# Kernel tuning notes

Hardware: AMD Instinct MI355X
Metric: run time of the kernel (lower is better)

## Reference

```python
import jax, jax.numpy as jnp
import numpy as np

N = 100000            # number of nodes
E = 1600000           # number of edges (avg degree 16)
D = 32                # embedding dim
MASK_DEPTH = 3        # cfg.mask_depth
PATH_PROB = 0.5       # cfg.path_prob
NUM_MASK_CAND = 1024  # cfg.num_mask_cand
EPS_NORM = 1e-12      # F.normalize eps


def setup_inputs() -> dict:
    key = jax.random.key(0)
    k1, k2 = jax.random.split(key)
    edge_index = jax.random.randint(k1, (2, E), 0, N)  # [2, E] (row, col) COO indices
    adj_values = jnp.ones((E,), dtype=jnp.float32)     # sparse values (binary adjacency)
    embeds = jax.random.normal(k2, (N, D), dtype=jnp.float32)
    return {"edge_index": edge_index, "adj_values": adj_values, "embeds": embeds}


def _spmm(rows, cols, vals, x):
    # out[i] = sum_{e: rows[e]==i} vals[e] * x[cols[e]]  -- irregular gather + scatter-add
    return jax.ops.segment_sum(x[cols] * vals[:, None], rows, num_segments=N)


def _l2_normalize(x):
    n = jnp.sqrt(jnp.sum(x * x, axis=-1, keepdims=True))
    return x / jnp.maximum(n, EPS_NORM)


def reference(edge_index, adj_values, embeds):
    rows, cols = edge_index[0], edge_index[1]
    vals = adj_values

    # order = row-sums of sparse adj, shape [N, 1]
    order = jax.ops.segment_sum(vals, rows, num_segments=N)[:, None]

    fst_emb = _spmm(rows, cols, vals, embeds) - embeds
    fst_num = order
    emb = [fst_emb]
    num = [fst_num]

    drop_key = jax.random.key(42)
    for i in range(MASK_DEPTH):
        # sparse_dropout with keep prob path_prob**(i+1); zeroing values == dropping edges in spmm
        keep_prob = PATH_PROB ** (i + 1)
        u = jax.random.uniform(jax.random.fold_in(drop_key, i), (E,))
        keep = jnp.floor(u + keep_prob)  # 1.0 with prob keep_prob, else 0.0
        vals = vals * keep               # dropout compounds across iterations

        emb.append(_spmm(rows, cols, vals, emb[-1]) - emb[-1] - order * emb[-1])
        num.append(_spmm(rows, cols, vals, num[-1]) - num[-1] - order)
        order = jax.ops.segment_sum(vals, rows, num_segments=N)[:, None]

    subgraph_embeds = sum(emb) / (sum(num) + 1e-8)
    subgraph_embeds = _l2_normalize(subgraph_embeds)
    embeds_n = _l2_normalize(embeds)

    scores = jnp.sum(subgraph_embeds * embeds_n, axis=-1)  # [N]
    # Gumbel noise: -log(-log(U))
    u = jax.random.uniform(jax.random.key(7), (N,))
    scores = scores + (-jnp.log(-jnp.log(u)))

    _, candidates = jax.lax.top_k(scores, NUM_MASK_CAND)
    return scores, candidates
```

## Files before the change

### kernel.cpp

```cpp
#include <hip/hip_runtime.h>
#include <stdint.h>
#include <stddef.h>

#define NN 100000
#define NE 1600000
#define DD 32
#define NCAND 1024
#define HSIZE 65536
#define SORTN 4096
#define NBUK ((NN + 255) / 256)
#define EPB 4096
#define BCAP 5120
#define BCAPL 4608
#define CHK 5

#define CAP1 832000
#define CAP2 432000
#define CAP3 240000

__host__ __device__ inline void tf2x32(uint32_t k0, uint32_t k1, uint32_t x0, uint32_t x1,
                                       uint32_t& o0, uint32_t& o1) {
  uint32_t ks2 = k0 ^ k1 ^ 0x1BD11BDAu;
  uint32_t v0 = x0 + k0, v1 = x1 + k1;
#define TFR(r) { v0 += v1; v1 = (v1 << (r)) | (v1 >> (32 - (r))); v1 ^= v0; }
  TFR(13) TFR(15) TFR(26) TFR(6)   v0 += k1;  v1 += ks2 + 1u;
  TFR(17) TFR(29) TFR(16) TFR(24)  v0 += ks2; v1 += k0 + 2u;
  TFR(13) TFR(15) TFR(26) TFR(6)   v0 += k0;  v1 += k1 + 3u;
  TFR(17) TFR(29) TFR(16) TFR(24)  v0 += k1;  v1 += ks2 + 4u;
  TFR(13) TFR(15) TFR(26) TFR(6)   v0 += ks2; v1 += k0 + 5u;
#undef TFR
  o0 = v0; o1 = v1;
}

__device__ __forceinline__ uint32_t jax_bits32(uint32_t k0, uint32_t k1, uint32_t i) {
  uint32_t o0, o1;
  tf2x32(k0, k1, 0u, i, o0, o1);
  return o0 ^ o1;
}

__device__ __forceinline__ float bits_to_uniform(uint32_t b) {
  return __fsub_rn(__uint_as_float((b >> 9) | 0x3f800000u), 1.0f);
}

__device__ __forceinline__ float pw32c(float4 c0, float4 c1, float4 c2, float4 c3,
                                       float4 c4, float4 c5, float4 c6, float4 c7) {
  float r0 = __fadd_rn(__fadd_rn(__fadd_rn(c0.x, c2.x), c4.x), c6.x);
  float r1 = __fadd_rn(__fadd_rn(__fadd_rn(c0.y, c2.y), c4.y), c6.y);
  float r2 = __fadd_rn(__fadd_rn(__fadd_rn(c0.z, c2.z), c4.z), c6.z);
  float r3 = __fadd_rn(__fadd_rn(__fadd_rn(c0.w, c2.w), c4.w), c6.w);
  float r4 = __fadd_rn(__fadd_rn(__fadd_rn(c1.x, c3.x), c5.x), c7.x);
  float r5 = __fadd_rn(__fadd_rn(__fadd_rn(c1.y, c3.y), c5.y), c7.y);
  float r6 = __fadd_rn(__fadd_rn(__fadd_rn(c1.z, c3.z), c5.z), c7.z);
  float r7 = __fadd_rn(__fadd_rn(__fadd_rn(c1.w, c3.w), c5.w), c7.w);
  float a01 = __fadd_rn(r0, r1), a23 = __fadd_rn(r2, r3);
  float a45 = __fadd_rn(r4, r5), a67 = __fadd_rn(r6, r7);
  return __fadd_rn(__fadd_rn(a01, a23), __fadd_rn(a45, a67));
}

__device__ __forceinline__ float4 f4div1(float4 a, float d) {
  return make_float4(__fdiv_rn(a.x, d), __fdiv_rn(a.y, d),
                     __fdiv_rn(a.z, d), __fdiv_rn(a.w, d));
}
__device__ __forceinline__ float4 f4sq(float4 a) {
  return make_float4(__fmul_rn(a.x, a.x), __fmul_rn(a.y, a.y),
                     __fmul_rn(a.z, a.z), __fmul_rn(a.w, a.w));
}
__device__ __forceinline__ float4 f4dd(float4 s, float n1, float4 e, float n2) {
  return make_float4(__fmul_rn(__fdiv_rn(s.x, n1), __fdiv_rn(e.x, n2)),
                     __fmul_rn(__fdiv_rn(s.y, n1), __fdiv_rn(e.y, n2)),
                     __fmul_rn(__fdiv_rn(s.z, n1), __fdiv_rn(e.z, n2)),
                     __fmul_rn(__fdiv_rn(s.w, n1), __fdiv_rn(e.w, n2)));
}

__global__ __launch_bounds__(1024) void kA2_bin(
    const int* __restrict__ rows, const int* __restrict__ cols,
    const float* __restrict__ adj,
    uint32_t k00, uint32_t k01, uint32_t k10, uint32_t k11,
    uint32_t k20, uint32_t k21,
    int* __restrict__ bucketCursor, int4* __restrict__ pkBin,
    int* __restrict__ bucketCntS) {
  __shared__ int hist[NBUK];
  __shared__ int base[NBUK];
  __shared__ int h1[NBUK];
  __shared__ int h2[NBUK];
  __shared__ int h3[NBUK];
  __shared__ uint8_t lvs[EPB];
  __shared__ uint16_t rank16[EPB];
  int tid = threadIdx.x;
  for (int i = tid; i < NBUK; i += 1024) { hist[i] = 0; h1[i] = 0; h2[i] = 0; h3[i] = 0; }
  __syncthreads();
  int e0 = blockIdx.x * EPB;
#pragma unroll
  for (int k = 0; k < 4; ++k) {
    int e = e0 + k * 1024 + tid;
    int lv = 0;
    if (e < NE) {
      float u0 = bits_to_uniform(jax_bits32(k00, k01, (uint32_t)e));
      float u1 = bits_to_uniform(jax_bits32(k10, k11, (uint32_t)e));
      float u2 = bits_to_uniform(jax_bits32(k20, k21, (uint32_t)e));
      float kp0 = floorf(__fadd_rn(u0, 0.5f));
      float kp1 = floorf(__fadd_rn(u1, 0.25f));
      float kp2 = floorf(__fadd_rn(u2, 0.125f));
      if (kp0 != 0.0f) { lv = 1; if (kp1 != 0.0f) { lv = 2; if (kp2 != 0.0f) lv = 3; } }
      int b = rows[e] >> 8;
      rank16[k * 1024 + tid] = (uint16_t)atomicAdd(&hist[b], 1);
      if (lv >= 1) {
        atomicAdd(&h1[b], 1);
        if (lv >= 2) {
          atomicAdd(&h2[b], 1);
          if (lv >= 3) atomicAdd(&h3[b], 1);
        }
      }
    }
    lvs[k * 1024 + tid] = (uint8_t)lv;
  }
  __syncthreads();
  for (int i = tid; i < NBUK; i += 1024) {
    int h = hist[i];
    base[i] = (h > 0) ? atomicAdd(&bucketCursor[i], h) : 0;
    if (h1[i]) atomicAdd(&bucketCntS[i], h1[i]);
    if (h2[i]) atomicAdd(&bucketCntS[NBUK + i], h2[i]);
    if (h3[i]) atomicAdd(&bucketCntS[2 * NBUK + i], h3[i]);
  }
  __syncthreads();
#pragma unroll
  for (int k = 0; k < 4; ++k) {
    int e = e0 + k * 1024 + tid;
    if (e < NE) {
      int r = rows[e];
      int b = r >> 8;
      int lv = (int)lvs[k * 1024 + tid];
      int pos = base[b] + (int)rank16[k * 1024 + tid];
      if (pos < BCAP)
        pkBin[(size_t)b * BCAP + pos] =
            make_int4(cols[e], __float_as_int(adj[e]), (e << 2) | lv, r);
    }
  }
}

__global__ __launch_bounds__(512) void k_scanBS(const int* __restrict__ bucketCursor,
                                                const int* __restrict__ bucketCntS,
                                                int* __restrict__ bucketBaseS) {
  __shared__ int sb[512];
  int a = blockIdx.x;
  const int* c = (a == 0) ? bucketCursor : (bucketCntS + (size_t)(a - 1) * NBUK);
  int* o = bucketBaseS + (size_t)a * (NBUK + 1);
  int tid = threadIdx.x;
  int v = (tid < NBUK) ? c[tid] : 0;
  sb[tid] = v;
  __syncthreads();
  for (int off = 1; off < 512; off <<= 1) {
    int x = (tid >= off) ? sb[tid - off] : 0;
    __syncthreads();
    sb[tid] += x;
    __syncthreads();
  }
  if (tid < NBUK) o[tid] = sb[tid] - v;
  if (tid == NBUK - 1) o[NBUK] = sb[tid];
}

__global__ __launch_bounds__(1024) void kB_emit(
    const int* __restrict__ bucketBaseS, const int4* __restrict__ pkBin,
    int* __restrict__ rpAll,
    int2* __restrict__ pk0, int2* __restrict__ pk1,
    int2* __restrict__ pk2, int2* __restrict__ pk3,
    float* __restrict__ order0, float* __restrict__ order1, float* __restrict__ order2) {
  __shared__ unsigned long long cnt64[256];
  __shared__ unsigned long long scan64[1024];
  __shared__ int start0[256];
  __shared__ int cur[256];
  __shared__ uint32_t keyF[BCAPL];
  __shared__ uint32_t keyG[BCAPL];
  __shared__ uint16_t origG[BCAPL];
  int b = blockIdx.x, tid = threadIdx.x;
  int bB0 = bucketBaseS[b];
  int n = bucketBaseS[b + 1] - bB0;
  if (n > BCAPL) n = BCAPL;
  size_t sRead = (size_t)b * BCAP;
  const int* pkI = (const int*)pkBin;
  const int2* pkZW = (const int2*)pkBin;
  int r0 = b << 8;
  int nr = NN - r0; if (nr > 256) nr = 256;
  int bB1 = bucketBaseS[(NBUK + 1) + b];
  int bB2 = bucketBaseS[2 * (NBUK + 1) + b];
  int bB3 = bucketBaseS[3 * (NBUK + 1) + b];
  if (tid < 256) { cnt64[tid] = 0ull; cur[tid] = 0; }
  __syncthreads();
  for (int i = tid; i < n; i += 1024) {
    int2 zw = pkZW[2 * (sRead + (size_t)i) + 1];
    int lr = zw.y - r0;
    int lv = zw.x & 3;
    keyF[i] = ((uint32_t)lr << 23) | (uint32_t)zw.x;
    unsigned long long add = 1ull;
    if (lv >= 1) add |= 1ull << 16;
    if (lv >= 2) add |= 1ull << 32;
    if (lv >= 3) add |= 1ull << 48;
    atomicAdd(&cnt64[lr], add);
  }
  __syncthreads();
  unsigned long long own = (tid < 256) ? cnt64[tid] : 0ull;
  if (tid < 256) scan64[tid] = own;
  __syncthreads();
  for (int off = 1; off < 256; off <<= 1) {
    unsigned long long v = (tid < 256 && tid >= off) ? scan64[tid - off] : 0ull;
    __syncthreads();
    if (tid < 256) scan64[tid] += v;
    __syncthreads();
  }
  if (tid < 256) {
    unsigned long long ex = scan64[tid] - own;
    start0[tid] = (int)(ex & 0xFFFFull);
    if (tid < nr) {
      rpAll[r0 + tid] = bB0 + (int)(ex & 0xFFFFull);
      rpAll[(NN + 1) + r0 + tid] = bB1 + (int)((ex >> 16) & 0xFFFFull);
      rpAll[2 * (NN + 1) + r0 + tid] = bB2 + (int)((ex >> 32) & 0xFFFFull);
      rpAll[3 * (NN + 1) + r0 + tid] = bB3 + (int)((ex >> 48) & 0xFFFFull);
    }
  }
  if (b == NBUK - 1 && tid == 0) {
    rpAll[NN] = bucketBaseS[NBUK];
    rpAll[(NN + 1) + NN] = bucketBaseS[(NBUK + 1) + NBUK];
    rpAll[2 * (NN + 1) + NN] = bucketBaseS[2 * (NBUK + 1) + NBUK];
    rpAll[3 * (NN + 1) + NN] = bucketBaseS[3 * (NBUK + 1) + NBUK];
  }
  __syncthreads();
  for (int i = tid; i < n; i += 1024) {
    uint32_t k = keyF[i];
    int lr = (int)(k >> 23);
    int slot = start0[lr] + atomicAdd(&cur[lr], 1);
    origG[slot] = (uint16_t)i;
    keyG[slot] = k;
  }
  __syncthreads();
  int C2 = (n + 1023) >> 10;
  {
    int lo2 = tid * C2, hi2 = lo2 + C2;
    if (lo2 > n) lo2 = n;
    if (hi2 > n) hi2 = n;
    uint16_t vals[CHK];
    uint16_t pos[CHK];
    uint32_t keys[CHK];
#pragma unroll
    for (int q = 0; q < CHK; ++q) {
      int i = lo2 + q;
      if (i < hi2) {
        uint32_t ki = keyG[i];
        int lr = (int)(ki >> 23);
        int st = start0[lr];
        int d = (int)(cnt64[lr] & 0xFFFFull);
        int rank = 0;
        for (int j = 0; j < d; ++j) rank += (keyG[st + j] < ki) ? 1 : 0;
        vals[q] = origG[i];
        keys[q] = ki;
        pos[q] = (uint16_t)(st + rank);
      }
    }
    __syncthreads();
#pragma unroll
    for (int q = 0; q < CHK; ++q) {
      int i = lo2 + q;
      if (i < hi2) { origG[pos[q]] = vals[q]; keyG[pos[q]] = keys[q]; }
    }
  }
  __syncthreads();
  uint32_t* adjS = keyF;
  {
    uint32_t av[CHK];
#pragma unroll
    for (int q = 0; q < CHK; ++q) {
      int i = tid + q * 1024;
      if (i < n) av[q] = (uint32_t)pkI[4 * (sRead + (size_t)origG[i]) + 1];
    }
#pragma unroll
    for (int q = 0; q < CHK; ++q) {
      int i = tid + q * 1024;
      if (i < n) adjS[i] = av[q];
    }
  }
  __syncthreads();
  if (tid < nr) {
    int d = (int)(cnt64[tid] & 0xFFFFull);
    int st = start0[tid];
    float o0 = 0.0f, o1v = 0.0f, o2v = 0.0f;
    for (int i = 0; i < d; ++i) {
      int lv = (int)(keyG[st + i] & 3u);
      float a = __uint_as_float(adjS[st + i]);
      o0 = __fadd_rn(o0, a);
      if (lv >= 1) { o1v = __fadd_rn(o1v, a); if (lv >= 2) o2v = __fadd_rn(o2v, a); }
    }
    order0[r0 + tid] = o0; order1[r0 + tid] = o1v; order2[r0 + tid] = o2v;
  }
  int lo = tid * C2, hi = lo + C2;
  if (lo > n) lo = n;
  if (hi > n) hi = n;
  int c1 = 0, c2 = 0, c3 = 0;
  for (int i = lo; i < hi; ++i) {
    int lv = (int)(keyG[i] & 3u);
    c1 += (lv >= 1); c2 += (lv >= 2); c3 += (lv >= 3);
  }
  unsigned long long mine = (unsigned long long)c1 |
                            ((unsigned long long)c2 << 16) |
                            ((unsigned long long)c3 << 32);
  scan64[tid] = mine;
  __syncthreads();
  for (int off = 1; off < 1024; off <<= 1) {
    unsigned long long v = (tid >= off) ? scan64[tid - off] : 0ull;
    __syncthreads();
    scan64[tid] += v;
    __syncthreads();
  }
  unsigned long long ex = scan64[tid] - mine;
  int o1 = bB1 + (int)(ex & 0xFFFFull);
  int o2 = bB2 + (int)((ex >> 16) & 0xFFFFull);
  int o3 = bB3 + (int)((ex >> 32) & 0xFFFFull);
  {
    int colr[CHK];
#pragma unroll
    for (int q = 0; q < CHK; ++q) {
      int i = lo + q;
      if (i < hi) colr[q] = pkI[4 * (sRead + (size_t)origG[i])];
    }
#pragma unroll
    for (int q = 0; q < CHK; ++q) {
      int i = lo + q;
      if (i < hi) {
        int lv = (int)(keyG[i] & 3u);
        int2 pkv = make_int2(colr[q], (int)adjS[i]);
        pk0[bB0 + i] = pkv;
        if (lv >= 1) {
          pk1[o1++] = pkv;
          if (lv >= 2) {
            pk2[o2++] = pkv;
            if (lv >= 3) pk3[o3++] = pkv;
          }
        }
      }
    }
  }
}


__global__ void k_emb0(const int* __restrict__ rp, const int2* __restrict__ pk,
                       const float* __restrict__ embeds, float* __restrict__ e0) {
  int tid = blockIdx.x * blockDim.x + threadIdx.x;
  int r = tid >> 5, d = tid & 31;
  if (r >= NN) return;
  int s = rp[r], t = rp[r + 1];
  float acc = 0.0f;
  for (int base = s; base < t; base += 32) {
    int idx = base + d;
    int2 p = (idx < t) ? pk[idx] : make_int2(0, 0);
    int m = t - base; if (m > 32) m = 32;
    for (int j = 0; j < m; j += 8) {
      int cc[8], aa[8];
      float xx[8];
#pragma unroll
      for (int q = 0; q < 8; ++q) {
        cc[q] = __shfl(p.x, j + q, 32);
        aa[q] = __shfl(p.y, j + q, 32);
      }
#pragma unroll
      for (int q = 0; q < 8; ++q) xx[q] = embeds[(size_t)cc[q] * DD + d];
#pragma unroll
      for (int q = 0; q < 8; ++q)
        acc = __fadd_rn(acc, __fmul_rn(__int_as_float(aa[q]), xx[q]));
    }
  }
  e0[(size_t)r * DD + d] = __fsub_rn(acc, embeds[(size_t)r * DD + d]);
}

__global__ void k_emb_step(const int* __restrict__ rp, const int2* __restrict__ pk,
                           const float* __restrict__ ord, const float* __restrict__ ecur,
                           float* __restrict__ enext, float* __restrict__ esum,
                           const float* __restrict__ ncur, float* __restrict__ nnext,
                           float* __restrict__ nsum, int mode) {
  int tid = blockIdx.x * blockDim.x + threadIdx.x;
  int r = tid >> 5, d = tid & 31;
  if (r >= NN) return;
  int s = rp[r], t = rp[r + 1];
  float acc = 0.0f, accn = 0.0f;
  for (int base = s; base < t; base += 32) {
    int idx = base + d;
    int2 p = (idx < t) ? pk[idx] : make_int2(0, 0);
    int m = t - base; if (m > 32) m = 32;
    for (int j = 0; j < m; j += 8) {
      int cc[8], aa[8];
      float xx[8], nn[8];
#pragma unroll
      for (int q = 0; q < 8; ++q) {
        cc[q] = __shfl(p.x, j + q, 32);
        aa[q] = __shfl(p.y, j + q, 32);
      }
#pragma unroll
      for (int q = 0; q < 8; ++q) {
        xx[q] = ecur[(size_t)cc[q] * DD + d];
        nn[q] = ncur[cc[q]];
      }
#pragma unroll
      for (int q = 0; q < 8; ++q) {
        float av = __int_as_float(aa[q]);
        acc = __fadd_rn(acc, __fmul_rn(av, xx[q]));
        accn = __fadd_rn(accn, __fmul_rn(av, nn[q]));
      }
    }
  }
  float ordv = ord[r];
  size_t idx = (size_t)r * DD + d;
  float ec = ecur[idx];
  float o = __fsub_rn(__fsub_rn(acc, ec), __fmul_rn(ordv, ec));
  if (mode != 3) enext[idx] = o;
  if (mode == 1) esum[idx] = __fadd_rn(ec, o);
  else esum[idx] = __fadd_rn(esum[idx], o);
  if (d == 0) {
    float nc = ncur[r];
    float on = __fsub_rn(__fsub_rn(accn, nc), ordv);
    if (mode != 3) nnext[r] = on;
    if (mode == 1) nsum[r] = __fadd_rn(nc, on);
    else nsum[r] = __fadd_rn(nsum[r], on);
  }
}

__global__ __launch_bounds__(256) void k_final(
    const float* __restrict__ embeds, const float* __restrict__ emb_sum,
    const float* __restrict__ num_sum, uint32_t gk0, uint32_t gk1,
    float* __restrict__ out_scores, int* __restrict__ hist) {
  __shared__ uint32_t hb[512];
  __shared__ uint32_t hc[512];
  int r = blockIdx.x * blockDim.x + threadIdx.x;
  for (int i = threadIdx.x; i < 512; i += 256) { hb[i] = 0xFFFFFFFFu; hc[i] = 0u; }
  __syncthreads();
  if (r < NN) {
    float denom = __fadd_rn(num_sum[r], 1e-8f);
    const float4* ps = (const float4*)(emb_sum + (size_t)r * DD);
    const float4* pe = (const float4*)(embeds + (size_t)r * DD);
    float4 m0 = pe[0], m1 = pe[1], m2 = pe[2], m3 = pe[3],
           m4 = pe[4], m5 = pe[5], m6 = pe[6], m7 = pe[7];
    float4 s0 = f4div1(ps[0], denom), s1 = f4div1(ps[1], denom),
           s2 = f4div1(ps[2], denom), s3 = f4div1(ps[3], denom),
           s4 = f4div1(ps[4], denom), s5 = f4div1(ps[5], denom),
           s6 = f4div1(ps[6], denom), s7 = f4div1(ps[7], denom);
    float n1 = fmaxf(__fsqrt_rn(pw32c(f4sq(s0), f4sq(s1), f4sq(s2), f4sq(s3),
                                      f4sq(s4), f4sq(s5), f4sq(s6), f4sq(s7))), 1e-12f);
    float n2 = fmaxf(__fsqrt_rn(pw32c(f4sq(m0), f4sq(m1), f4sq(m2), f4sq(m3),
                                      f4sq(m4), f4sq(m5), f4sq(m6), f4sq(m7))), 1e-12f);
    float dot = pw32c(f4dd(s0, n1, m0, n2), f4dd(s1, n1, m1, n2),
                      f4dd(s2, n1, m2, n2), f4dd(s3, n1, m3, n2),
                      f4dd(s4, n1, m4, n2), f4dd(s5, n1, m5, n2),
                      f4dd(s6, n1, m6, n2), f4dd(s7, n1, m7, n2));
    float u = bits_to_uniform(jax_bits32(gk0, gk1, (uint32_t)r));
    float l1 = (float)log((double)u);
    float w = -l1;
    float l2 = (float)log((double)w);
    float g = -l2;
    float score = __fadd_rn(dot, g);
    out_scores[r] = score;
    uint32_t kb = __float_as_uint(score);
    kb = (kb & 0x80000000u) ? ~kb : (kb | 0x80000000u);
    uint32_t key = kb >> 16;
    uint32_t slot = (key * 2654435761u) >> 23;
    for (;;) {
      uint32_t prev = atomicCAS(&hb[slot], 0xFFFFFFFFu, key);
      if (prev == 0xFFFFFFFFu || prev == key) { atomicAdd(&hc[slot], 1u); break; }
      slot = (slot + 1) & 511u;
    }
  }
  __syncthreads();
  for (int i = threadIdx.x; i < 512; i += 256)
    if (hb[i] != 0xFFFFFFFFu) atomicAdd(&hist[hb[i]], (int)hc[i]);
}

__global__ void k_cutoff(const int* __restrict__ hist, int* __restrict__ cutoff) {
  __shared__ int psum[1024];
  int t = threadIdx.x;
  int base = HSIZE - (t + 1) * 64;
  int own = 0;
  for (int i = 0; i < 64; ++i) own += hist[base + i];
  psum[t] = own;
  __syncthreads();
  for (int off = 1; off < 1024; off <<= 1) {
    int v = (t >= off) ? psum[t - off] : 0;
    __syncthreads();
    psum[t] += v;
    __syncthreads();
  }
  int incl = psum[t];
  int prev = incl - own;
  if (incl >= NCAND && prev < NCAND) {
    int c = prev;
    int b = HSIZE - t * 64 - 1;
    while (b >= base) {
      c += hist[b];
      if (c >= NCAND) break;
      --b;
    }
    *cutoff = b;
  }
}

__global__ void k_collect(const float* __restrict__ scores, const int* __restrict__ cutoff,
                          unsigned long long* __restrict__ buf, int* __restrict__ cnt2) {
  int r = blockIdx.x * blockDim.x + threadIdx.x;
  if (r >= NN) return;
  uint32_t kb = __float_as_uint(scores[r]);
  kb = (kb & 0x80000000u) ? ~kb : (kb | 0x80000000u);
  if ((int)(kb >> 16) >= *cutoff) {
    int p = atomicAdd(cnt2, 1);
    if (p < SORTN)
      buf[p] = ((unsigned long long)kb << 32) | (uint32_t)(~(uint32_t)r);
  }
}

__global__ __launch_bounds__(256) void k_rank(const unsigned long long* __restrict__ buf,
                                              const int* __restrict__ cnt2,
                                              float* __restrict__ out_cand) {
  __shared__ unsigned long long s[SORTN];
  int m = *cnt2;
  if (m > SORTN) m = SORTN;
  if (blockIdx.x * 256 >= m) return;
  for (int i = threadIdx.x; i < m; i += 256) s[i] = buf[i];
  __syncthreads();
  int i = blockIdx.x * 256 + threadIdx.x;
  if (i >= m) return;
  unsigned long long mine = s[i];
  int rank = 0;
  int j = 0;
  for (; j + 8 <= m; j += 8) {
#pragma unroll
    for (int q = 0; q < 8; ++q) rank += (s[j + q] > mine) ? 1 : 0;
  }
  for (; j < m; ++j) rank += (s[j] > mine) ? 1 : 0;
  if (rank < NCAND) {
    uint32_t idx = ~((uint32_t)(mine & 0xffffffffull));
    out_cand[rank] = (float)idx;
  }
}

extern "C" void kernel_launch(void* const* d_in, const int* in_sizes, int n_in,
                              void* d_out, int out_size, void* d_ws, size_t ws_size,
                              hipStream_t stream) {
  const int* rows = (const int*)d_in[0];
  const int* cols = rows + NE;
  const float* adj = (const float*)d_in[1];
  const float* embeds = (const float*)d_in[2];
  float* out = (float*)d_out;

  char* p = (char*)d_ws;
  auto alloc = [&](size_t bytes) {
    char* q = p;
    p += (bytes + 255) & ~(size_t)255;
    return q;
  };
  size_t zero_bytes = (size_t)(4 * NBUK + HSIZE + 8) * 4;
  char* zero_base = (char*)alloc(zero_bytes);
  int* bucketCursor = (int*)zero_base;
  int* bucketCntS = bucketCursor + NBUK;
  int* hist = bucketCntS + 3 * NBUK;
  int* cnt2 = hist + HSIZE;

  int* bucketBaseS = (int*)alloc((size_t)4 * (NBUK + 1) * 4);
  int* rpAll = (int*)alloc((size_t)4 * (NN + 1) * 4);
  size_t padBytes = (size_t)NBUK * BCAP * 16;
  char* unionAB = (char*)alloc(padBytes);
  int4* pkBin = (int4*)unionAB;
  float* embA = (float*)unionAB;
  float* embB = (float*)(unionAB + (size_t)NN * DD * 4);
  int2* pk0 = (int2*)alloc((size_t)NE * 8);
  int2* pk1 = (int2*)alloc((size_t)CAP1 * 8);
  int2* pk2 = (int2*)alloc((size_t)CAP2 * 8);
  int2* pk3 = (int2*)alloc((size_t)CAP3 * 8);
  float* embS = (float*)alloc((size_t)NN * DD * 4);
  float* order0 = (float*)alloc(NN * 4);
  float* order1 = (float*)alloc(NN * 4);
  float* order2 = (float*)alloc(NN * 4);
  float* num1 = (float*)alloc(NN * 4);
  float* num2 = (float*)alloc(NN * 4);
  float* numS = (float*)alloc(NN * 4);
  unsigned long long* buf = (unsigned long long*)alloc(SORTN * 8);

  uint32_t dk[3][2];
  for (int i = 0; i < 3; ++i) tf2x32(0u, 42u, 0u, (uint32_t)i, dk[i][0], dk[i][1]);

  hipMemsetAsync(zero_base, 0, zero_bytes, stream);

  int gE = (NE + EPB - 1) / EPB;
  kA2_bin<<<gE, 1024, 0, stream>>>(rows, cols, adj, dk[0][0], dk[0][1], dk[1][0], dk[1][1],
                                   dk[2][0], dk[2][1], bucketCursor, pkBin, bucketCntS);
  k_scanBS<<<4, 512, 0, stream>>>(bucketCursor, bucketCntS, bucketBaseS);
  kB_emit<<<NBUK, 1024, 0, stream>>>(bucketBaseS, pkBin, rpAll,
                                     pk0, pk1, pk2, pk3, order0, order1, order2);

  const int* rp0 = rpAll;
  const int* rp1 = rpAll + (NN + 1);
  const int* rp2 = rpAll + 2 * (NN + 1);
  const int* rp3 = rpAll + 3 * (NN + 1);

  int gEmb = (NN * 32 + 255) / 256;
  k_emb0<<<gEmb, 256, 0, stream>>>(rp0, pk0, embeds, embA);

  k_emb_step<<<gEmb, 256, 0, stream>>>(rp1, pk1, order0, embA, embB, embS,
                                       order0, num1, numS, 1);
  k_emb_step<<<gEmb, 256, 0, stream>>>(rp2, pk2, order1, embB, embA, embS,
                                       num1, num2, numS, 2);
  k_emb_step<<<gEmb, 256, 0, stream>>>(rp3, pk3, order2, embA, embB, embS,
                                       num2, num1, numS, 3);

  k_final<<<(NN + 255) / 256, 256, 0, stream>>>(embeds, embS, numS, 0u, 7u, out, hist);
  k_cutoff<<<1, 1024, 0, stream>>>(hist, cnt2 + 1);
  k_collect<<<(NN + 255) / 256, 256, 0, stream>>>(out, cnt2 + 1, buf, cnt2);
  k_rank<<<(SORTN + 255) / 256, 256, 0, stream>>>(buf, cnt2, out + NN);
}
```

Baseline: 345.6 us.

## Stage score inputs through LDS for coalesced loads and split histogram kernel

The final scoring kernel now loads emb_sum and embeds with coalesced float4 reads into a padded shared-memory tile, replacing per-thread strided row loads, then computes norms, dot product and Gumbel noise from LDS. The radix histogram moves into a separate 1024-thread kernel with a larger per-block hash table, so fewer blocks issue global atomics. This adds one kernel launch and a re-read of the score array, and the staging needs extra barriers and LDS traffic.

```diff
diff --git a/kernel.cpp b/kernel.cpp
--- a/kernel.cpp
+++ b/kernel.cpp
@@ -420,53 +420,99 @@
   }
 }
 
-__global__ __launch_bounds__(256) void k_final(
+__global__ __launch_bounds__(256) void k_score(
     const float* __restrict__ embeds, const float* __restrict__ emb_sum,
     const float* __restrict__ num_sum, uint32_t gk0, uint32_t gk1,
-    float* __restrict__ out_scores, int* __restrict__ hist) {
-  __shared__ uint32_t hb[512];
-  __shared__ uint32_t hc[512];
-  int r = blockIdx.x * blockDim.x + threadIdx.x;
-  for (int i = threadIdx.x; i < 512; i += 256) { hb[i] = 0xFFFFFFFFu; hc[i] = 0u; }
+    float* __restrict__ out_scores) {
+  __shared__ float sm[256 * 33];
+  int t = threadIdx.x;
+  int b = blockIdx.x;
+  int f4base = b * 2048;
+  const float4* gS = (const float4*)emb_sum;
+  const float4* gE = (const float4*)embeds;
+#pragma unroll
+  for (int k = 0; k < 8; ++k) {
+    int loc = k * 256 + t;
+    int g = f4base + loc;
+    if (g < NN * 8) {
+      int row = loc >> 3, c4 = loc & 7;
+      float4 v = gS[g];
+      float* d1 = &sm[row * 33 + c4 * 4];
+      d1[0] = v.x; d1[1] = v.y; d1[2] = v.z; d1[3] = v.w;
+    }
+  }
+  __syncthreads();
+  int r = b * 256 + t;
+  int rc = (r < NN) ? r : 0;
+  float denom = __fadd_rn(num_sum[rc], 1e-8f);
+  const float* rs = &sm[t * 33];
+  float4 s0 = f4div1(make_float4(rs[0], rs[1], rs[2], rs[3]), denom);
+  float4 s1 = f4div1(make_float4(rs[4], rs[5], rs[6], rs[7]), denom);
+  float4 s2 = f4div1(make_float4(rs[8], rs[9], rs[10], rs[11]), denom);
+  float4 s3 = f4div1(make_float4(rs[12], rs[13], rs[14], rs[15]), denom);
+  float4 s4 = f4div1(make_float4(rs[16], rs[17], rs[18], rs[19]), denom);
+  float4 s5 = f4div1(make_float4(rs[20], rs[21], rs[22], rs[23]), denom);
+  float4 s6 = f4div1(make_float4(rs[24], rs[25], rs[26], rs[27]), denom);
+  float4 s7 = f4div1(make_float4(rs[28], rs[29], rs[30], rs[31]), denom);
+  float n1 = fmaxf(__fsqrt_rn(pw32c(f4sq(s0), f4sq(s1), f4sq(s2), f4sq(s3),
+                                    f4sq(s4), f4sq(s5), f4sq(s6), f4sq(s7))), 1e-12f);
+  __syncthreads();
+#pragma unroll
+  for (int k = 0; k < 8; ++k) {
+    int loc = k * 256 + t;
+    int g = f4base + loc;
+    if (g < NN * 8) {
+      int row = loc >> 3, c4 = loc & 7;
+      float4 w = gE[g];
+      float* d2 = &sm[row * 33 + c4 * 4];
+      d2[0] = w.x; d2[1] = w.y; d2[2] = w.z; d2[3] = w.w;
+    }
+  }
+  __syncthreads();
+  float4 m0 = make_float4(rs[0], rs[1], rs[2], rs[3]);
+  float4 m1 = make_float4(rs[4], rs[5], rs[6], rs[7]);
+  float4 m2 = make_float4(rs[8], rs[9], rs[10], rs[11]);
+  float4 m3 = make_float4(rs[12], rs[13], rs[14], rs[15]);
+  float4 m4 = make_float4(rs[16], rs[17], rs[18], rs[19]);
+  float4 m5 = make_float4(rs[20], rs[21], rs[22], rs[23]);
+  float4 m6 = make_float4(rs[24], rs[25], rs[26], rs[27]);
+  float4 m7 = make_float4(rs[28], rs[29], rs[30], rs[31]);
+  float n2 = fmaxf(__fsqrt_rn(pw32c(f4sq(m0), f4sq(m1), f4sq(m2), f4sq(m3),
+                                    f4sq(m4), f4sq(m5), f4sq(m6), f4sq(m7))), 1e-12f);
+  float dot = pw32c(f4dd(s0, n1, m0, n2), f4dd(s1, n1, m1, n2),
+                    f4dd(s2, n1, m2, n2), f4dd(s3, n1, m3, n2),
+                    f4dd(s4, n1, m4, n2), f4dd(s5, n1, m5, n2),
+                    f4dd(s6, n1, m6, n2), f4dd(s7, n1, m7, n2));
+  float u = bits_to_uniform(jax_bits32(gk0, gk1, (uint32_t)rc));
+  float l1 = (float)log((double)u);
+  float w = -l1;
+  float l2 = (float)log((double)w);
+  float g = -l2;
+  if (r < NN) out_scores[r] = __fadd_rn(dot, g);
+}
+
+__global__ __launch_bounds__(1024) void k_hist(const float* __restrict__ scores,
+                                               int* __restrict__ hist) {
+  __shared__ uint32_t hb[1024];
+  __shared__ uint32_t hc[1024];
+  int t = threadIdx.x;
+  int r = blockIdx.x * 1024 + t;
+  hb[t] = 0xFFFFFFFFu;
+  hc[t] = 0u;
   __syncthreads();
   if (r < NN) {
-    float denom = __fadd_rn(num_sum[r], 1e-8f);
-    const float4* ps = (const float4*)(emb_sum + (size_t)r * DD);
-    const float4* pe = (const float4*)(embeds + (size_t)r * DD);
-    float4 m0 = pe[0], m1 = pe[1], m2 = pe[2], m3 = pe[3],
-           m4 = pe[4], m5 = pe[5], m6 = pe[6], m7 = pe[7];
-    float4 s0 = f4div1(ps[0], denom), s1 = f4div1(ps[1], denom),
-           s2 = f4div1(ps[2], denom), s3 = f4div1(ps[3], denom),
-           s4 = f4div1(ps[4], denom), s5 = f4div1(ps[5], denom),
-           s6 = f4div1(ps[6], denom), s7 = f4div1(ps[7], denom);
-    float n1 = fmaxf(__fsqrt_rn(pw32c(f4sq(s0), f4sq(s1), f4sq(s2), f4sq(s3),
-                                      f4sq(s4), f4sq(s5), f4sq(s6), f4sq(s7))), 1e-12f);
-    float n2 = fmaxf(__fsqrt_rn(pw32c(f4sq(m0), f4sq(m1), f4sq(m2), f4sq(m3),
-                                      f4sq(m4), f4sq(m5), f4sq(m6), f4sq(m7))), 1e-12f);
-    float dot = pw32c(f4dd(s0, n1, m0, n2), f4dd(s1, n1, m1, n2),
-                      f4dd(s2, n1, m2, n2), f4dd(s3, n1, m3, n2),
-                      f4dd(s4, n1, m4, n2), f4dd(s5, n1, m5, n2),
-                      f4dd(s6, n1, m6, n2), f4dd(s7, n1, m7, n2));
-    float u = bits_to_uniform(jax_bits32(gk0, gk1, (uint32_t)r));
-    float l1 = (float)log((double)u);
-    float w = -l1;
-    float l2 = (float)log((double)w);
-    float g = -l2;
-    float score = __fadd_rn(dot, g);
-    out_scores[r] = score;
-    uint32_t kb = __float_as_uint(score);
+    uint32_t kb = __float_as_uint(scores[r]);
     kb = (kb & 0x80000000u) ? ~kb : (kb | 0x80000000u);
     uint32_t key = kb >> 16;
-    uint32_t slot = (key * 2654435761u) >> 23;
+    uint32_t slot = (key * 2654435761u) >> 22;
     for (;;) {
       uint32_t prev = atomicCAS(&hb[slot], 0xFFFFFFFFu, key);
       if (prev == 0xFFFFFFFFu || prev == key) { atomicAdd(&hc[slot], 1u); break; }
-      slot = (slot + 1) & 511u;
-    }
-  }
-  __syncthreads();
-  for (int i = threadIdx.x; i < 512; i += 256)
-    if (hb[i] != 0xFFFFFFFFu) atomicAdd(&hist[hb[i]], (int)hc[i]);
+      slot = (slot + 1) & 1023u;
+    }
+  }
+  __syncthreads();
+  if (hb[t] != 0xFFFFFFFFu) atomicAdd(&hist[hb[t]], (int)hc[t]);
 }
 
 __global__ void k_cutoff(const int* __restrict__ hist, int* __restrict__ cutoff) {
@@ -604,7 +650,8 @@
   k_emb_step<<<gEmb, 256, 0, stream>>>(rp3, pk3, order2, embA, embB, embS,
                                        num2, num1, numS, 3);
 
-  k_final<<<(NN + 255) / 256, 256, 0, stream>>>(embeds, embS, numS, 0u, 7u, out, hist);
+  k_score<<<(NN + 255) / 256, 256, 0, stream>>>(embeds, embS, numS, 0u, 7u, out);
+  k_hist<<<(NN + 1023) / 1024, 1024, 0, stream>>>(out, hist);
   k_cutoff<<<1, 1024, 0, stream>>>(hist, cnt2 + 1);
   k_collect<<<(NN + 255) / 256, 256, 0, stream>>>(out, cnt2 + 1, buf, cnt2);
   k_rank<<<(SORTN + 255) / 256, 256, 0, stream>>>(buf, cnt2, out + NN);
```

Result: faster. 334.4 us, median of 2 (-3.2%).
